# Optimization experiments

Measured on AMD Instinct MI355X. Metric: run time of the kernel, lower is better.

The kernel has to match this reference:

```python
import jax, jax.numpy as jnp
import numpy as np
import math

# ---- static configuration (mirrors Renderer defaults) ----
S = 129                                 # density cube side
L = math.ceil(S * math.sqrt(3))         # padded/rotation cube side = 224
C_ABS = 0.2                             # absorption coefficient c
LIGHTS = [
    {'dir': (2, 1, 1),    'rgb': (1.0, 69.0 / 255.0, 25.0 / 255.0)},
    {'dir': (-1, 0.5, 0), 'rgb': (227.0 / 255.0, 1.0, 66.0 / 255.0)},
]


def yp_from_light(l):
    ld = np.asarray(l, dtype=np.float64)
    ld = ld / np.sqrt(np.sum(ld ** 2))
    y = -math.asin(ld[0])
    if ld[2] < 0:
        y = -math.pi - y
    y = y * 180.0 / math.pi
    p = math.asin(ld[1]) * 180.0 / math.pi
    return y, p


def rot_matrix(yaw_deg, pitch_deg, order):
    # yaw about the y (height) axis, pitch about the x axis, roll = 0
    y = math.radians(yaw_deg)
    p = math.radians(pitch_deg)
    Ry = np.array([[math.cos(y), 0.0, math.sin(y)],
                   [0.0, 1.0, 0.0],
                   [-math.sin(y), 0.0, math.cos(y)]], dtype=np.float32)
    Rp = np.array([[1.0, 0.0, 0.0],
                   [0.0, math.cos(p), -math.sin(p)],
                   [0.0, math.sin(p), math.cos(p)]], dtype=np.float32)
    return Ry @ Rp if order == 'ypr' else Rp @ Ry

# base normalized sampling grid (align_corners=True convention), (x,y,z) order
_lin = np.linspace(-1.0, 1.0, L, dtype=np.float32)
_zz, _yy, _xx = np.meshgrid(_lin, _lin, _lin, indexing='ij')
BASE_XYZ = np.stack([_xx, _yy, _zz], axis=-1)   # [L,L,L,3]


def rotate_volume(vol, R):
    """Trilinear resampling of vol [B,C,D,H,W] under rotation R (zero padding)."""
    B, Ch, D, H, W = vol.shape
    src = jnp.einsum('dhwc,kc->dhwk', jnp.asarray(BASE_XYZ), jnp.asarray(R))
    xs = (src[..., 0] + 1.0) * 0.5 * (W - 1)
    ys = (src[..., 1] + 1.0) * 0.5 * (H - 1)
    zs = (src[..., 2] + 1.0) * 0.5 * (D - 1)
    x0 = jnp.floor(xs).astype(jnp.int32)
    y0 = jnp.floor(ys).astype(jnp.int32)
    z0 = jnp.floor(zs).astype(jnp.int32)
    wx = (xs - x0).astype(vol.dtype)
    wy = (ys - y0).astype(vol.dtype)
    wz = (zs - z0).astype(vol.dtype)
    flat = vol.reshape(B, Ch, D * H * W)

    def gather(zi, yi, xi):
        inb = ((zi >= 0) & (zi < D) & (yi >= 0) & (yi < H) & (xi >= 0) & (xi < W)).astype(vol.dtype)
        idx = ((jnp.clip(zi, 0, D - 1) * H + jnp.clip(yi, 0, H - 1)) * W
               + jnp.clip(xi, 0, W - 1)).reshape(-1)
        return jnp.take(flat, idx, axis=2).reshape(B, Ch, D, H, W) * inb

    out = (gather(z0,     y0,     x0)     * ((1 - wz) * (1 - wy) * (1 - wx))
         + gather(z0,     y0,     x0 + 1) * ((1 - wz) * (1 - wy) * wx)
         + gather(z0,     y0 + 1, x0)     * ((1 - wz) * wy * (1 - wx))
         + gather(z0,     y0 + 1, x0 + 1) * ((1 - wz) * wy * wx)
         + gather(z0 + 1, y0,     x0)     * (wz * (1 - wy) * (1 - wx))
         + gather(z0 + 1, y0,     x0 + 1) * (wz * (1 - wy) * wx)
         + gather(z0 + 1, y0 + 1, x0)     * (wz * wy * (1 - wx))
         + gather(z0 + 1, y0 + 1, x0 + 1) * (wz * wy * wx))
    return out


def _revcumsum(a):
    # torch.flip(cumsum(flip(a,[2]),2),[2]) : reverse cumulative sum along depth
    return jnp.flip(jnp.cumsum(jnp.flip(a, 2), axis=2), 2)


def setup_inputs() -> dict:
    key = jax.random.key(0)
    d = jax.random.uniform(key, (1, 1, S, S, S), dtype=jnp.float32)
    return {'d': d}


def reference(d):
    bs, _, Sd, _, _ = d.shape
    i = L // 2 - Sd // 2
    j = i + Sd
    light_array = jnp.zeros((bs, 3, Sd, Sd, Sd), dtype=d.dtype)
    for l in LIGHTS:
        y, p = yp_from_light(l['dir'])
        up = jnp.zeros((bs, 1, L, L, L), dtype=d.dtype).at[:, :, i:j, i:j, i:j].set(d)
        up = rotate_volume(up, rot_matrix(y, p, 'ypr'))
        up = jnp.exp(-C_ABS * _revcumsum(up))           # transmittance toward light
        up = rotate_volume(up, rot_matrix(-y, -p, 'rpy'))
        color = jnp.asarray(l['rgb'], dtype=d.dtype).reshape(1, 3, 1, 1, 1)
        light_array = light_array + up[:, :, i:j, i:j, i:j] * color
    t = jnp.exp(-C_ABS * _revcumsum(d))                  # view-ray transmittance
    out = C_ABS * jnp.sum(d * light_array * t, axis=2)   # background = 0
    return jnp.clip(out, 0.0, 1.0)
```

## Files before the change

kernel.cpp:

```cpp
#include <hip/hip_runtime.h>
#include <hip/hip_fp16.h>
#include <math.h>

#ifndef M_PI
#define M_PI 3.14159265358979323846
#endif

#define SS   129
#define LL   224
#define LL2  (LL*LL)
#define LL3  (LL*LL*LL)
#define SS2  (SS*SS)
#define SS3  (SS*SS*SS)
#define CABS 0.2f
#define PAD  48

#define BLO 45.5f
#define BHI 178.5f

#define NT1  28
#define NTZ16 14
#define ROTG  (2 * NTZ16 * 784)
#define ROTCH 392
#define NT3  17
#define NBZ16 9
#define BACKG (2 * NBZ16 * 289)
#define BACKCH 17
#define BACKG_P 5304
#define NTZ  28

#define NSEG 16
#define SEGZ 9
#define DSEGT (NSEG * SS2)
#define EXB1 ((DSEGT + 511) / 512)
#define EXB2 4
#define ROTG_E (ROTG + EXB1 + EXB2)
#define PREB1 ((DSEGT + 255) / 256)
#define SUFG (392 + PREB1)
#define TEXPB (2 * NTZ * LL2 / 2 / 256)

#define RBX 21
#define RBY 16
#define RBZ 18
#define RBN (RBX*RBY*RBZ)
#define RSXZ (RBX*RBZ)

#define BBX 21
#define BBY 16
#define BBZ 19
#define BBN (BBX*BBY*BBZ)
#define BSXZ (BBX*BBZ)

struct Mat3 { float m[9]; };
struct F3   { float x, y, z; };

__device__ __forceinline__ F3 tile_center(const Mat3& M, int ox, int oy, int oz) {
    float cbx = fmaf((float)ox + 3.5f, 2.0f / 223.0f, -1.0f);
    float cby = fmaf((float)oy + 3.5f, 2.0f / 223.0f, -1.0f);
    float cbz = fmaf((float)oz + 3.5f, 2.0f / 223.0f, -1.0f);
    F3 qc;
    qc.x = fmaf(fmaf(M.m[0], cbx, fmaf(M.m[1], cby, M.m[2] * cbz)), 111.5f, 111.5f);
    qc.y = fmaf(fmaf(M.m[3], cbx, fmaf(M.m[4], cby, M.m[5] * cbz)), 111.5f, 111.5f);
    qc.z = fmaf(fmaf(M.m[6], cbx, fmaf(M.m[7], cby, M.m[8] * cbz)), 111.5f, 111.5f);
    return qc;
}

__device__ __forceinline__ F3 tile_center16(const Mat3& M, int ox, int oy, int oz) {
    float cbx = fmaf((float)ox + 3.5f, 2.0f / 223.0f, -1.0f);
    float cby = fmaf((float)oy + 3.5f, 2.0f / 223.0f, -1.0f);
    float cbz = fmaf((float)oz + 7.5f, 2.0f / 223.0f, -1.0f);
    F3 qc;
    qc.x = fmaf(fmaf(M.m[0], cbx, fmaf(M.m[1], cby, M.m[2] * cbz)), 111.5f, 111.5f);
    qc.y = fmaf(fmaf(M.m[3], cbx, fmaf(M.m[4], cby, M.m[5] * cbz)), 111.5f, 111.5f);
    qc.z = fmaf(fmaf(M.m[6], cbx, fmaf(M.m[7], cby, M.m[8] * cbz)), 111.5f, 111.5f);
    return qc;
}

__device__ __forceinline__ bool tile_accept(F3 qc, F3 H) {
    return !(qc.x + H.x < BLO || qc.x - H.x > BHI ||
             qc.y + H.y < BLO || qc.y - H.y > BHI ||
             qc.z + H.z < BLO || qc.z - H.z > BHI);
}

__device__ __forceinline__ void qmap(const Mat3& M, int x, int y, int z,
                                     float& qx, float& qy, float& qz) {
    float bx = fmaf((float)x, 2.0f / 223.0f, -1.0f);
    float by = fmaf((float)y, 2.0f / 223.0f, -1.0f);
    float bz = fmaf((float)z, 2.0f / 223.0f, -1.0f);
    qx = fmaf(fmaf(M.m[0], bx, fmaf(M.m[1], by, M.m[2] * bz)), 111.5f, 111.5f);
    qy = fmaf(fmaf(M.m[3], bx, fmaf(M.m[4], by, M.m[5] * bz)), 111.5f, 111.5f);
    qz = fmaf(fmaf(M.m[6], bx, fmaf(M.m[7], by, M.m[8] * bz)), 111.5f, 111.5f);
}

__device__ __forceinline__ float fetch_d(const float* __restrict__ d, int z, int y, int x) {
    unsigned zz = (unsigned)(z - PAD), yy = (unsigned)(y - PAD), xx = (unsigned)(x - PAD);
    return (zz < (unsigned)SS && yy < (unsigned)SS && xx < (unsigned)SS)
        ? d[((int)zz * SS + (int)yy) * SS + (int)xx] : 0.0f;
}

__device__ __forceinline__ float fetch_T(const float* __restrict__ T, int z, int y, int x) {
    unsigned zz = (unsigned)z, yy = (unsigned)y, xx = (unsigned)x;
    return (zz < (unsigned)LL && yy < (unsigned)LL && xx < (unsigned)LL)
        ? T[((int)zz * LL + (int)yy) * LL + (int)xx] : 0.0f;
}

__device__ __forceinline__ float tri_T(const float* __restrict__ T, float qz, float qy, float qx) {
    int x0 = (int)floorf(qx), y0 = (int)floorf(qy), z0 = (int)floorf(qz);
    float wx = qx - (float)x0, wy = qy - (float)y0, wz = qz - (float)z0;
    float c000 = fetch_T(T, z0, y0, x0),     c001 = fetch_T(T, z0, y0, x0 + 1);
    float c010 = fetch_T(T, z0, y0 + 1, x0), c011 = fetch_T(T, z0, y0 + 1, x0 + 1);
    float c100 = fetch_T(T, z0 + 1, y0, x0),     c101 = fetch_T(T, z0 + 1, y0, x0 + 1);
    float c110 = fetch_T(T, z0 + 1, y0 + 1, x0), c111 = fetch_T(T, z0 + 1, y0 + 1, x0 + 1);
    float a00 = c000 + wx * (c001 - c000), a01 = c010 + wx * (c011 - c010);
    float a10 = c100 + wx * (c101 - c100), a11 = c110 + wx * (c111 - c110);
    float b0 = a00 + wy * (a01 - a00), b1 = a10 + wy * (a11 - a10);
    return b0 + wz * (b1 - b0);
}

__device__ __forceinline__ float tri_d_g(const float* __restrict__ d, float qz, float qy, float qx) {
    int x0 = (int)floorf(qx), y0 = (int)floorf(qy), z0 = (int)floorf(qz);
    float wx = qx - (float)x0, wy = qy - (float)y0, wz = qz - (float)z0;
    float c000 = fetch_d(d, z0, y0, x0),     c001 = fetch_d(d, z0, y0, x0 + 1);
    float c010 = fetch_d(d, z0, y0 + 1, x0), c011 = fetch_d(d, z0, y0 + 1, x0 + 1);
    float c100 = fetch_d(d, z0 + 1, y0, x0),     c101 = fetch_d(d, z0 + 1, y0, x0 + 1);
    float c110 = fetch_d(d, z0 + 1, y0 + 1, x0), c111 = fetch_d(d, z0 + 1, y0 + 1, x0 + 1);
    float a00 = c000 + wx * (c001 - c000), a01 = c010 + wx * (c011 - c010);
    float a10 = c100 + wx * (c101 - c100), a11 = c110 + wx * (c111 - c110);
    float b0 = a00 + wy * (a01 - a00), b1 = a10 + wy * (a11 - a10);
    return b0 + wz * (b1 - b0);
}

__device__ __forceinline__ float tri_rot(const float* __restrict__ S,
                                         float qx, float qy, float qz,
                                         int lox, int loy, int loz) {
    int x0 = (int)floorf(qx), y0 = (int)floorf(qy), z0 = (int)floorf(qz);
    float wx = qx - (float)x0, wy = qy - (float)y0, wz = qz - (float)z0;
    int i = (y0 - loy) * 378 + (z0 - loz) * 21 + (x0 - lox);
    float c000 = S[i],        c001 = S[i + 1];
    float cz0  = S[i + 21],   cz1  = S[i + 22];
    float cy0  = S[i + 378],  cy1  = S[i + 379];
    float cw0  = S[i + 399],  cw1  = S[i + 400];
    float a00 = c000 + wx * (c001 - c000);
    float a01 = cy0  + wx * (cy1  - cy0);
    float a10 = cz0  + wx * (cz1  - cz0);
    float a11 = cw0  + wx * (cw1  - cw0);
    float b0  = a00 + wy * (a01 - a00);
    float b1  = a10 + wy * (a11 - a10);
    return b0 + wz * (b1 - b0);
}

__device__ __forceinline__ float tri_back(const float* __restrict__ S,
                                          float qx, float qy, float qz,
                                          int lox, int loy, int loz) {
    int x0 = (int)floorf(qx), y0 = (int)floorf(qy), z0 = (int)floorf(qz);
    float wx = qx - (float)x0, wy = qy - (float)y0, wz = qz - (float)z0;
    int i = (y0 - loy) * 399 + (z0 - loz) * 21 + (x0 - lox);
    float c000 = S[i],        c001 = S[i + 1];
    float cz0  = S[i + 21],   cz1  = S[i + 22];
    float cy0  = S[i + 399],  cy1  = S[i + 400];
    float cw0  = S[i + 420],  cw1  = S[i + 421];
    float a00 = c000 + wx * (c001 - c000);
    float a01 = cy0  + wx * (cy1  - cy0);
    float a10 = cz0  + wx * (cz1  - cz0);
    float a11 = cw0  + wx * (cw1  - cw0);
    float b0  = a00 + wy * (a01 - a00);
    float b1  = a10 + wy * (a11 - a10);
    return b0 + wz * (b1 - b0);
}

__global__ __launch_bounds__(512) void k_rot(const float* __restrict__ d,
        __half* __restrict__ T0, __half* __restrict__ T1,
        float* __restrict__ S0, float* __restrict__ S1,
        float* __restrict__ Dseg, float* __restrict__ A,
        unsigned short* __restrict__ Run,
        Mat3 M0, Mat3 M1, F3 H0, F3 H1, F3 G0, F3 G1) {
    int n = blockIdx.x;
    int tid = threadIdx.x;
    if (n >= ROTG) {
        int e = n - ROTG;
        if (e < EXB1) {
            int t = e * 512 + tid;
            if (t < 2 * SS2) A[t] = 0.0f;
            if (t >= DSEGT) return;
            int seg = t / SS2, col = t - seg * SS2;
            int zs = seg * SEGZ, ze = min(SS, zs + SEGZ);
            float run = 0.0f;
            for (int z = zs; z < ze; ++z) run += d[z * SS2 + col];
            Dseg[t] = run;
        } else {
            int id = (e - EXB1) * 512 + tid;
            if (id >= 2 * 784) return;
            int l = id / 784, r = id - l * 784;
            int ty = r / 28, tx = r - ty * 28;
            const Mat3 M = l ? M1 : M0;
            const F3  G  = l ? G1 : G0;
            int t0 = -1, t1 = -1;
            for (int tz = 0; tz < NT1; ++tz) {
                F3 qc = tile_center(M, tx * 8, ty * 8, tz * 8);
                if (tile_accept(qc, G)) { if (t0 < 0) t0 = tz; t1 = tz; }
            }
            Run[id] = (t0 < 0) ? 0xFFFFu : (unsigned short)(t0 | (t1 << 8));
        }
        return;
    }

    int x8 = n & 7, i8 = n >> 3;
    int c = i8 / ROTCH, off = i8 - c * ROTCH;
    int b = (c * 8 + x8) * ROTCH + off;

    int light = b / (NTZ16 * 784);
    int r = b - light * (NTZ16 * 784);
    int tz16 = r / 784;
    int r2 = r - tz16 * 784;
    int tty = r2 / 28, ttx = r2 - tty * 28;

    const Mat3 M = light ? M1 : M0;
    const F3  H  = light ? H1 : H0;
    __half* __restrict__ T   = light ? T1 : T0;
    float* __restrict__ Ssum = light ? S1 : S0;

    int ox = ttx * 8, oy = tty * 8, oz = tz16 * 16;
    F3 qc = tile_center16(M, ox, oy, oz);
    if (!tile_accept(qc, H)) return;

    int lox = (int)floorf(qc.x - H.x);
    int loy = (int)floorf(qc.y - H.y);
    int loz = (int)floorf(qc.z - H.z);

    __shared__ float S[RBN];
    __shared__ float Sc[1024];

    if (tid < RSXZ) {
        int ix = tid % RBX, iz = tid / RBX;
        bool interior = (lox >= PAD) & (lox <= PAD + SS - RBX) &
                        (loy >= PAD) & (loy <= PAD + SS - RBY) &
                        (loz >= PAD) & (loz <= PAD + SS - RBZ);
        if (interior) {
            const float* g = d + ((size_t)(loz + iz - PAD) * SS + (loy - PAD)) * SS
                               + (lox + ix - PAD);
            #pragma unroll
            for (int j = 0; j < RBY; ++j)
                S[tid + j * RSXZ] = g[j * SS];
        } else {
            #pragma unroll
            for (int j = 0; j < RBY; ++j)
                S[tid + j * RSXZ] = fetch_d(d, loz + iz, loy + j, lox + ix);
        }
    }
    __syncthreads();

    int lx = tid & 7, ly = (tid >> 3) & 7, lz = tid >> 6;
    int col = tid & 63;
    float fx = (float)lx - 3.5f, fy = (float)ly - 3.5f, fz = (float)lz - 7.5f;
    float qx = qc.x + fmaf(M.m[0], fx, fmaf(M.m[1], fy, M.m[2] * fz));
    float qy = qc.y + fmaf(M.m[3], fx, fmaf(M.m[4], fy, M.m[5] * fz));
    float qz = qc.z + fmaf(M.m[6], fx, fmaf(M.m[7], fy, M.m[8] * fz));
    float v0 = tri_rot(S, qx, qy, qz, lox, loy, loz);
    float qx2 = qx + 8.0f * M.m[2];
    float qy2 = qy + 8.0f * M.m[5];
    float qz2 = qz + 8.0f * M.m[8];
    float v1 = tri_rot(S, qx2, qy2, qz2, lox, loy, loz);

    Sc[lz * 64 + col] = v0;
    Sc[(lz + 8) * 64 + col] = v1;
    __syncthreads();
    if (tid < 128) {
        int zz = tid >> 3, ly2 = tid & 7;
        const float4* Sc4 = (const float4*)Sc;
        float4 f0 = Sc4[zz * 16 + ly2 * 2];
        float4 f1 = Sc4[zz * 16 + ly2 * 2 + 1];
        union { __half2 h[4]; float4 v; } u;
        u.h[0] = __floats2half2_rn(f0.x, f0.y);
        u.h[1] = __floats2half2_rn(f0.z, f0.w);
        u.h[2] = __floats2half2_rn(f1.x, f1.y);
        u.h[3] = __floats2half2_rn(f1.z, f1.w);
        *(float4*)&T[(size_t)(oz + zz) * LL2 + (oy + ly2) * LL + ox] = u.v;
    } else if (tid < 256) {
        int t2 = tid - 128;
        int cc = t2 & 63, h = t2 >> 6;
        float s = 0.0f;
        #pragma unroll
        for (int k = 0; k < 8; ++k) s += Sc[(h * 8 + k) * 64 + cc];
        int so = (oy + (cc >> 3)) * LL + (ox + (cc & 7));
        Ssum[(2 * tz16 + h) * LL2 + so] = s;
    }
}

__global__ __launch_bounds__(256) void k_sufw(float* __restrict__ S0,
        float* __restrict__ S1, const unsigned short* __restrict__ Run,
        const float* __restrict__ d, const float* __restrict__ Dseg,
        __half* __restrict__ W) {
    int b = blockIdx.x;
    if (b < 392) {
        int l = b / 196;
        int col = (b - l * 196) * 256 + threadIdx.x;
        float* __restrict__ Ssum = l ? S1 : S0;
        int x = col % LL, y = col / LL;
        unsigned short r = Run[l * 784 + (y >> 3) * 28 + (x >> 3)];
        if (r == 0xFFFFu) return;
        int t0 = r & 0xFF, t1 = r >> 8;
        float vbuf[NTZ];
        #pragma unroll
        for (int t = 0; t < NTZ; ++t)
            vbuf[t] = (t >= t0 && t <= t1) ? Ssum[t * LL2 + col] : 0.0f;
        float run = 0.0f;
        #pragma unroll
        for (int t = NTZ - 1; t >= 0; --t) {
            if (t >= t0 && t <= t1) Ssum[t * LL2 + col] = run;
            run += vbuf[t];
        }
    } else {
        int t = (b - 392) * 256 + threadIdx.x;
        if (t >= DSEGT) return;
        int seg = t / SS2, col = t - seg * SS2;
        int zs = seg * SEGZ, ze = min(SS, zs + SEGZ);
        float run = 0.0f;
        for (int s2 = seg + 1; s2 < NSEG; ++s2) run += Dseg[s2 * SS2 + col];
        for (int z = ze - 1; z >= zs; --z) {
            float dv = d[z * SS2 + col];
            run += dv;
            W[z * SS2 + col] = __float2half(dv * __expf(-CABS * run));
        }
    }
}

__global__ __launch_bounds__(256) void k_texp(__half* __restrict__ T0,
        __half* __restrict__ T1, const float* __restrict__ S0,
        const float* __restrict__ S1, const unsigned short* __restrict__ Run) {
    int id = blockIdx.x * 256 + threadIdx.x;
    int light = id / (NTZ * LL2 / 2);
    int r = id - light * (NTZ * LL2 / 2);
    int t = r / (LL2 / 2), cp = r - t * (LL2 / 2);
    int col = cp * 2;
    int y = col / LL, x = col - y * LL;
    const unsigned short* Rl = Run + light * 784 + (y >> 3) * 28;
    unsigned short rtA = Rl[x >> 3];
    unsigned short rtB = Rl[(x + 1) >> 3];
    bool aA = (rtA != 0xFFFFu) && t >= (rtA & 0xFF) && t <= (rtA >> 8);
    bool aB = (rtB != 0xFFFFu) && t >= (rtB & 0xFF) && t <= (rtB >> 8);
    if (!aA && !aB) return;
    const float* __restrict__ Ssum = light ? S1 : S0;
    __half* __restrict__ T = light ? T1 : T0;
    float offA = aA ? Ssum[t * LL2 + col]     : 0.0f;
    float offB = aB ? Ssum[t * LL2 + col + 1] : 0.0f;
    __half2* Tp = (__half2*)(T + (size_t)(8 * t) * LL2 + col);
    float2 v[8];
    #pragma unroll
    for (int k = 0; k < 8; ++k) v[k] = __half22float2(Tp[k * (LL2 / 2)]);
    float sA = 0.0f, sB = 0.0f;
    #pragma unroll
    for (int k = 7; k >= 0; --k) { sA += v[k].x; sB += v[k].y; v[k].x = sA; v[k].y = sB; }
    #pragma unroll
    for (int k = 0; k < 8; ++k) {
        float eA = aA ? __expf(-CABS * (v[k].x + offA)) : v[k].x;
        float eB = aB ? __expf(-CABS * (v[k].y + offB)) : v[k].y;
        Tp[k * (LL2 / 2)] = __floats2half2_rn(eA, eB);
    }
}

template<bool BINT>
__global__ __launch_bounds__(512) void k_back(const __half* __restrict__ T0,
        const __half* __restrict__ T1, const __half* __restrict__ W,
        float* __restrict__ A0, float* __restrict__ A1,
        Mat3 M0, Mat3 M1, F3 H0, F3 H1) {
    int n = blockIdx.x;
    int x8 = n & 7, i8 = n >> 3;
    int c = i8 / BACKCH, off = i8 - c * BACKCH;
    int lb = (c * 8 + x8) * BACKCH + off;
    if (lb >= BACKG) return;

    int light = lb / (NBZ16 * 289); lb -= light * (NBZ16 * 289);
    int tz16 = lb / 289;
    int r2 = lb - tz16 * 289;
    int tty = r2 / 17, ttx = r2 - tty * 17;

    const Mat3 M = light ? M1 : M0;
    const F3  H  = light ? H1 : H0;
    const __half* __restrict__ T = light ? T1 : T0;
    float* __restrict__ A = light ? A1 : A0;

    int ox = ttx * 8, oy = tty * 8, oz = tz16 * 16;
    F3 qc = tile_center16(M, ox + PAD, oy + PAD, oz + PAD);
    int lox = (int)floorf(qc.x - H.x);
    int loy = (int)floorf(qc.y - H.y);
    int loz = (int)floorf(qc.z - H.z);

    __shared__ float S[BBN];
    __shared__ float Sc[512];
    int tid = threadIdx.x;

    if (tid < BSXZ) {
        int ix = tid % BBX, iz = tid / BBX;
        if (BINT) {
            const __half* tb = T + ((size_t)(loz + iz) * LL + loy) * LL + (lox + ix);
            #pragma unroll
            for (int j = 0; j < BBY; ++j)
                S[tid + j * BSXZ] = __half2float(tb[j * LL]);
        } else {
            #pragma unroll
            for (int j = 0; j < BBY; ++j) {
                int gz = loz + iz, gy = loy + j, gx = lox + ix;
                bool inb = ((unsigned)gz < (unsigned)LL) & ((unsigned)gy < (unsigned)LL)
                         & ((unsigned)gx < (unsigned)LL);
                S[tid + j * BSXZ] = inb
                    ? __half2float(T[((size_t)gz * LL + gy) * LL + gx]) : 0.0f;
            }
        }
    }
    __syncthreads();

    int lx = tid & 7, ly = (tid >> 3) & 7, lz = tid >> 6;
    int col = tid & 63;
    int x = ox + lx, y = oy + ly;
    float v0 = 0.0f, v1 = 0.0f;
    if (x < SS && y < SS) {
        float fx = (float)lx - 3.5f, fy = (float)ly - 3.5f, fz = (float)lz - 7.5f;
        float qx = qc.x + fmaf(M.m[0], fx, fmaf(M.m[1], fy, M.m[2] * fz));
        float qy = qc.y + fmaf(M.m[3], fx, fmaf(M.m[4], fy, M.m[5] * fz));
        float qz = qc.z + fmaf(M.m[6], fx, fmaf(M.m[7], fy, M.m[8] * fz));
        int z0 = oz + lz, z1 = oz + 8 + lz;
        if (z0 < SS)
            v0 = tri_back(S, qx, qy, qz, lox, loy, loz)
               * __half2float(W[(z0 * SS + y) * SS + x]);
        if (z1 < SS) {
            float qx2 = qx + 8.0f * M.m[2];
            float qy2 = qy + 8.0f * M.m[5];
            float qz2 = qz + 8.0f * M.m[8];
            v1 = tri_back(S, qx2, qy2, qz2, lox, loy, loz)
               * __half2float(W[(z1 * SS + y) * SS + x]);
        }
    }
    Sc[lz * 64 + col] = v0 + v1;
    __syncthreads();
    if (tid < 64) {
        float s = 0.0f;
        #pragma unroll
        for (int k = 0; k < 8; ++k) s += Sc[k * 64 + tid];
        int xx = ox + (tid & 7), yy = oy + (tid >> 3);
        if (xx < SS && yy < SS) atomicAdd(&A[yy * SS + xx], s);
    }
}

__global__ __launch_bounds__(256) void k_combine(const float* __restrict__ A0,
        const float* __restrict__ A1, float* __restrict__ out, F3 c0, F3 c1) {
    int i = blockIdx.x * 256 + threadIdx.x;
    if (i >= 3 * SS2) return;
    int ch = i / SS2, col = i - ch * SS2;
    float r0 = (ch == 0) ? c0.x : ((ch == 1) ? c0.y : c0.z);
    float r1 = (ch == 0) ? c1.x : ((ch == 1) ? c1.y : c1.z);
    float o = CABS * (A0[col] * r0 + A1[col] * r1);
    out[i] = fminf(fmaxf(o, 0.0f), 1.0f);
}

__global__ __launch_bounds__(256) void k_rot_full(const float* __restrict__ d,
                                                  float* __restrict__ T, Mat3 R) {
    int i = blockIdx.x * 256 + threadIdx.x;
    if (i >= LL3) return;
    int x = i % LL; int r = i / LL; int y = r % LL; int z = r / LL;
    float qx, qy, qz; qmap(R, x, y, z, qx, qy, qz);
    T[i] = tri_d_g(d, qz, qy, qx);
}

__global__ __launch_bounds__(256) void k_scan_full(float* __restrict__ T) {
    int col = blockIdx.x * 256 + threadIdx.x;
    if (col >= LL2) return;
    float run = 0.0f;
    for (int z = LL - 1; z >= 0; --z) {
        int idx = z * LL2 + col;
        run += T[idx];
        T[idx] = __expf(-CABS * run);
    }
}

__global__ __launch_bounds__(64) void k_fused_back(const float* __restrict__ T,
        const float* __restrict__ d, float* __restrict__ LA, Mat3 RT,
        float cr, float cg, float cb, int first) {
    int col = blockIdx.x * 64 + threadIdx.x;
    if (col >= SS2) return;
    int y = col / SS, x = col % SS;
    float run = 0.0f, acc = 0.0f;
    for (int z = SS - 1; z >= 0; --z) {
        float qx, qy, qz; qmap(RT, x + PAD, y + PAD, z + PAD, qx, qy, qz);
        float u = tri_T(T, qz, qy, qx);
        float dv = d[z * SS2 + col];
        run += dv;
        acc = fmaf(dv * __expf(-CABS * run), u, acc);
    }
    if (first) {
        LA[0 * SS2 + col] = acc * cr;
        LA[1 * SS2 + col] = acc * cg;
        LA[2 * SS2 + col] = acc * cb;
    } else {
        LA[0 * SS2 + col] += acc * cr;
        LA[1 * SS2 + col] += acc * cg;
        LA[2 * SS2 + col] += acc * cb;
    }
}

__global__ __launch_bounds__(256) void k_clip(const float* __restrict__ LA,
                                              float* __restrict__ out) {
    int i = blockIdx.x * 256 + threadIdx.x;
    if (i < 3 * SS2) out[i] = fminf(fmaxf(CABS * LA[i], 0.0f), 1.0f);
}

static void light_mats(const double ld_in[3], Mat3& R, Mat3& RT) {
    double n = sqrt(ld_in[0]*ld_in[0] + ld_in[1]*ld_in[1] + ld_in[2]*ld_in[2]);
    double l0 = ld_in[0]/n, l1 = ld_in[1]/n, l2 = ld_in[2]/n;
    double yv = -asin(l0);
    if (l2 < 0) yv = -M_PI - yv;
    double yd = yv * 180.0 / M_PI, pd = asin(l1) * 180.0 / M_PI;
    double yr = yd * M_PI / 180.0, pr = pd * M_PI / 180.0;
    float cy = (float)cos(yr), sy = (float)sin(yr), cp = (float)cos(pr), sp = (float)sin(pr);
    float m[9] = { cy,  sy*sp,  sy*cp,
                   0.f, cp,    -sp,
                  -sy,  cy*sp,  cy*cp };
    for (int i = 0; i < 9; ++i) R.m[i] = m[i];
    RT.m[0] = m[0]; RT.m[1] = m[3]; RT.m[2] = m[6];
    RT.m[3] = m[1]; RT.m[4] = m[4]; RT.m[5] = m[7];
    RT.m[6] = m[2]; RT.m[7] = m[5]; RT.m[8] = m[8];
}

static F3 half_span8(const Mat3& M) {
    F3 h;
    h.x = 3.5f * (fabsf(M.m[0]) + fabsf(M.m[1]) + fabsf(M.m[2])) + 0.05f;
    h.y = 3.5f * (fabsf(M.m[3]) + fabsf(M.m[4]) + fabsf(M.m[5])) + 0.05f;
    h.z = 3.5f * (fabsf(M.m[6]) + fabsf(M.m[7]) + fabsf(M.m[8])) + 0.05f;
    return h;
}

static F3 half_span16(const Mat3& M) {
    F3 h;
    h.x = 3.5f * (fabsf(M.m[0]) + fabsf(M.m[1])) + 7.5f * fabsf(M.m[2]) + 0.1f;
    h.y = 3.5f * (fabsf(M.m[3]) + fabsf(M.m[4])) + 7.5f * fabsf(M.m[5]) + 0.1f;
    h.z = 3.5f * (fabsf(M.m[6]) + fabsf(M.m[7])) + 7.5f * fabsf(M.m[8]) + 0.1f;
    return h;
}

static void h_qc16(const Mat3& M, double ox, double oy, double oz, double q[3]) {
    double cb[3] = { (ox + 3.5) * 2.0 / 223.0 - 1.0,
                     (oy + 3.5) * 2.0 / 223.0 - 1.0,
                     (oz + 7.5) * 2.0 / 223.0 - 1.0 };
    for (int k = 0; k < 3; ++k)
        q[k] = ((double)M.m[3*k] * cb[0] + (double)M.m[3*k+1] * cb[1]
              + (double)M.m[3*k+2] * cb[2]) * 111.5 + 111.5;
}

extern "C" void kernel_launch(void* const* d_in, const int* in_sizes, int n_in,
                              void* d_out, int out_size, void* d_ws, size_t ws_size,
                              hipStream_t stream) {
    const float* d = (const float*)d_in[0];
    float* out = (float*)d_out;

    const double dirs[2][3] = { {2.0, 1.0, 1.0}, {-1.0, 0.5, 0.0} };
    F3 c0 = { 1.0f, 69.0f / 255.0f, 25.0f / 255.0f };
    F3 c1 = { 227.0f / 255.0f, 1.0f, 66.0f / 255.0f };
    Mat3 R[2], RT[2];
    light_mats(dirs[0], R[0], RT[0]);
    light_mats(dirs[1], R[1], RT[1]);
    F3 H8[2]  = { half_span8(R[0]),  half_span8(R[1])  };
    F3 H16[2] = { half_span16(R[0]), half_span16(R[1]) };
    F3 HB[2]  = { half_span16(RT[0]), half_span16(RT[1]) };

    bool bint = true;
    for (int l = 0; l < 2 && bint; ++l) {
        double H[3] = { HB[l].x, HB[l].y, HB[l].z };
        int dim[3] = { BBX, BBY, BBZ };
        for (int tz = 0; tz < NBZ16 && bint; ++tz)
            for (int ty = 0; ty < NT3 && bint; ++ty)
                for (int tx = 0; tx < NT3; ++tx) {
                    double q[3]; h_qc16(RT[l], tx * 8 + PAD, ty * 8 + PAD, tz * 16 + PAD, q);
                    for (int k = 0; k < 3; ++k) {
                        int lo = (int)floor(q[k] - H[k]);
                        if (lo < 1 || lo + dim[k] > LL - 1) { bint = false; break; }
                    }
                    if (!bint) break;
                }
    }

    const size_t f32n = (size_t)(2 * NTZ * LL2 + NSEG * SS2 + 2 * SS2);
    const size_t need_A = f32n * 4 + (size_t)(SS3 + 2 * LL3) * 2 + 2 * 784 * 2;
    const size_t need_C = (size_t)(LL3 + 3 * SS2) * 4;

    if (ws_size >= need_A) {
        float* S0   = (float*)d_ws;
        float* S1   = S0 + NTZ * LL2;
        float* Dseg = S1 + NTZ * LL2;
        float* A0   = Dseg + NSEG * SS2;
        float* A1   = A0 + SS2;
        __half* W   = (__half*)(A1 + SS2);
        __half* T0  = W + SS3;
        __half* T1  = T0 + LL3;
        unsigned short* Run = (unsigned short*)(T1 + LL3);

        k_rot  <<<ROTG_E, 512, 0, stream>>>(d, T0, T1, S0, S1, Dseg, A0, Run,
                                            R[0], R[1], H16[0], H16[1], H8[0], H8[1]);
        k_sufw <<<SUFG, 256, 0, stream>>>(S0, S1, Run, d, Dseg, W);
        k_texp <<<TEXPB, 256, 0, stream>>>(T0, T1, S0, S1, Run);
        if (bint)
            k_back<true><<<BACKG_P, 512, 0, stream>>>(T0, T1, W, A0, A1,
                                                      RT[0], RT[1], HB[0], HB[1]);
        else
            k_back<false><<<BACKG_P, 512, 0, stream>>>(T0, T1, W, A0, A1,
                                                       RT[0], RT[1], HB[0], HB[1]);
        k_combine<<<(3 * SS2 + 255) / 256, 256, 0, stream>>>(A0, A1, out, c0, c1);
    } else if (ws_size >= need_C) {
        float* T  = (float*)d_ws;
        float* LA = T + LL3;
        for (int l = 0; l < 2; ++l) {
            k_rot_full <<<(LL3 + 255) / 256, 256, 0, stream>>>(d, T, R[l]);
            k_scan_full<<<(LL2 + 255) / 256, 256, 0, stream>>>(T);
            k_fused_back<<<(SS2 + 63) / 64, 64, 0, stream>>>(T, d, LA, RT[l],
                l ? c1.x : c0.x, l ? c1.y : c0.y, l ? c1.z : c0.z, l == 0);
        }
        k_clip<<<(3 * SS2 + 255) / 256, 256, 0, stream>>>(LA, out);
    }
}
```

Baseline: 166.0 us.

## Fuse pipeline into one cooperative persistent kernel with grid syncs

Replaces the five separate launches (rotate, suffix sums, texp, back-projection, combine) with a single cooperative kernel that uses grid-wide syncs between stages and persistent blocks looping over work. It aims to remove per-launch overhead and inter-kernel gaps. The trade-off is that occupancy is capped by cooperative residency, the block-to-tile mapping loses the earlier swizzled ordering, and the shared-memory footprint becomes the max across stages. The sufw scan loop is also simplified to iterate only the active tile range.

```diff
diff --git a/kernel.cpp b/kernel.cpp
--- a/kernel.cpp
+++ b/kernel.cpp
@@ -1,6 +1,9 @@
 #include <hip/hip_runtime.h>
 #include <hip/hip_fp16.h>
+#include <hip/hip_cooperative_groups.h>
 #include <math.h>
+
+namespace cg = cooperative_groups;
 
 #ifndef M_PI
 #define M_PI 3.14159265358979323846
@@ -166,6 +169,275 @@
     float b0  = a00 + wy * (a01 - a00);
     float b1  = a10 + wy * (a11 - a10);
     return b0 + wz * (b1 - b0);
+}
+
+__global__ __launch_bounds__(512) void k_all(const float* __restrict__ d,
+        __half* __restrict__ T0, __half* __restrict__ T1,
+        float* __restrict__ S0, float* __restrict__ S1,
+        float* __restrict__ Dseg, float* __restrict__ A0, float* __restrict__ A1,
+        __half* __restrict__ W, unsigned short* __restrict__ Run,
+        float* __restrict__ out,
+        Mat3 M0, Mat3 M1, Mat3 P0, Mat3 P1,
+        F3 H0, F3 H1, F3 G0, F3 G1, F3 B0, F3 B1,
+        F3 c0, F3 c1, int bint) {
+    cg::grid_group gg = cg::this_grid();
+    const int tid  = threadIdx.x;
+    const int nb   = gridDim.x;
+    const int gtid = blockIdx.x * 512 + tid;
+    const int gth  = nb * 512;
+
+    __shared__ float S[BBN];
+    __shared__ float Sc[1024];
+
+    for (int t = gtid; t < 2 * SS2; t += gth) A0[t] = 0.0f;
+    for (int t = gtid; t < DSEGT; t += gth) {
+        int seg = t / SS2, col = t - seg * SS2;
+        int zs = seg * SEGZ, ze = min(SS, zs + SEGZ);
+        float run = 0.0f;
+        for (int z = zs; z < ze; ++z) run += d[z * SS2 + col];
+        Dseg[t] = run;
+    }
+    for (int id = gtid; id < 2 * 784; id += gth) {
+        int l = id / 784, r = id - l * 784;
+        int ty = r / 28, tx = r - ty * 28;
+        const Mat3 M = l ? M1 : M0;
+        const F3  G  = l ? G1 : G0;
+        int t0 = -1, t1 = -1;
+        for (int tz = 0; tz < NT1; ++tz) {
+            F3 qc = tile_center(M, tx * 8, ty * 8, tz * 8);
+            if (tile_accept(qc, G)) { if (t0 < 0) t0 = tz; t1 = tz; }
+        }
+        Run[id] = (t0 < 0) ? 0xFFFFu : (unsigned short)(t0 | (t1 << 8));
+    }
+
+    {
+        int bch = (ROTG + nb - 1) / nb;
+        int base = blockIdx.x * bch;
+        for (int k = 0; k < bch; ++k) {
+            int b = base + k;
+            if (b >= ROTG) break;
+            int light = b / (NTZ16 * 784);
+            int r = b - light * (NTZ16 * 784);
+            int tz16 = r / 784;
+            int r2 = r - tz16 * 784;
+            int tty = r2 / 28, ttx = r2 - tty * 28;
+
+            const Mat3 M = light ? M1 : M0;
+            const F3  H  = light ? H1 : H0;
+            __half* __restrict__ T   = light ? T1 : T0;
+            float* __restrict__ Ssum = light ? S1 : S0;
+
+            int ox = ttx * 8, oy = tty * 8, oz = tz16 * 16;
+            F3 qc = tile_center16(M, ox, oy, oz);
+            if (!tile_accept(qc, H)) continue;
+
+            int lox = (int)floorf(qc.x - H.x);
+            int loy = (int)floorf(qc.y - H.y);
+            int loz = (int)floorf(qc.z - H.z);
+
+            if (tid < RSXZ) {
+                int ix = tid % RBX, iz = tid / RBX;
+                bool interior = (lox >= PAD) & (lox <= PAD + SS - RBX) &
+                                (loy >= PAD) & (loy <= PAD + SS - RBY) &
+                                (loz >= PAD) & (loz <= PAD + SS - RBZ);
+                if (interior) {
+                    const float* g = d + ((size_t)(loz + iz - PAD) * SS + (loy - PAD)) * SS
+                                       + (lox + ix - PAD);
+                    #pragma unroll
+                    for (int j = 0; j < RBY; ++j)
+                        S[tid + j * RSXZ] = g[j * SS];
+                } else {
+                    #pragma unroll
+                    for (int j = 0; j < RBY; ++j)
+                        S[tid + j * RSXZ] = fetch_d(d, loz + iz, loy + j, lox + ix);
+                }
+            }
+            __syncthreads();
+
+            int lx = tid & 7, ly = (tid >> 3) & 7, lz = tid >> 6;
+            int col = tid & 63;
+            float fx = (float)lx - 3.5f, fy = (float)ly - 3.5f, fz = (float)lz - 7.5f;
+            float qx = qc.x + fmaf(M.m[0], fx, fmaf(M.m[1], fy, M.m[2] * fz));
+            float qy = qc.y + fmaf(M.m[3], fx, fmaf(M.m[4], fy, M.m[5] * fz));
+            float qz = qc.z + fmaf(M.m[6], fx, fmaf(M.m[7], fy, M.m[8] * fz));
+            float v0 = tri_rot(S, qx, qy, qz, lox, loy, loz);
+            float qx2 = qx + 8.0f * M.m[2];
+            float qy2 = qy + 8.0f * M.m[5];
+            float qz2 = qz + 8.0f * M.m[8];
+            float v1 = tri_rot(S, qx2, qy2, qz2, lox, loy, loz);
+
+            Sc[lz * 64 + col] = v0;
+            Sc[(lz + 8) * 64 + col] = v1;
+            __syncthreads();
+            if (tid < 128) {
+                int zz = tid >> 3, ly2 = tid & 7;
+                const float4* Sc4 = (const float4*)Sc;
+                float4 f0 = Sc4[zz * 16 + ly2 * 2];
+                float4 f1 = Sc4[zz * 16 + ly2 * 2 + 1];
+                union { __half2 h[4]; float4 v; } u;
+                u.h[0] = __floats2half2_rn(f0.x, f0.y);
+                u.h[1] = __floats2half2_rn(f0.z, f0.w);
+                u.h[2] = __floats2half2_rn(f1.x, f1.y);
+                u.h[3] = __floats2half2_rn(f1.z, f1.w);
+                *(float4*)&T[(size_t)(oz + zz) * LL2 + (oy + ly2) * LL + ox] = u.v;
+            } else if (tid < 256) {
+                int t2 = tid - 128;
+                int cc = t2 & 63, h = t2 >> 6;
+                float s = 0.0f;
+                #pragma unroll
+                for (int kk = 0; kk < 8; ++kk) s += Sc[(h * 8 + kk) * 64 + cc];
+                int so = (oy + (cc >> 3)) * LL + (ox + (cc & 7));
+                Ssum[(2 * tz16 + h) * LL2 + so] = s;
+            }
+            __syncthreads();
+        }
+    }
+    gg.sync();
+
+    for (int i = gtid; i < 2 * LL2; i += gth) {
+        int l = i / LL2, col = i - l * LL2;
+        float* __restrict__ Ssum = l ? S1 : S0;
+        int x = col % LL, y = col / LL;
+        unsigned short r = Run[l * 784 + (y >> 3) * 28 + (x >> 3)];
+        if (r == 0xFFFFu) continue;
+        int t0 = r & 0xFF, t1 = r >> 8;
+        float run = 0.0f;
+        for (int t = t1; t >= t0; --t) {
+            float v = Ssum[t * LL2 + col];
+            Ssum[t * LL2 + col] = run;
+            run += v;
+        }
+    }
+    for (int t = gtid; t < DSEGT; t += gth) {
+        int seg = t / SS2, col = t - seg * SS2;
+        int zs = seg * SEGZ, ze = min(SS, zs + SEGZ);
+        float run = 0.0f;
+        for (int s2 = seg + 1; s2 < NSEG; ++s2) run += Dseg[s2 * SS2 + col];
+        for (int z = ze - 1; z >= zs; --z) {
+            float dv = d[z * SS2 + col];
+            run += dv;
+            W[z * SS2 + col] = __float2half(dv * __expf(-CABS * run));
+        }
+    }
+    gg.sync();
+
+    for (int id = gtid; id < NTZ * LL2; id += gth) {
+        int light = id / (NTZ * LL2 / 2);
+        int r = id - light * (NTZ * LL2 / 2);
+        int t = r / (LL2 / 2), cp = r - t * (LL2 / 2);
+        int col = cp * 2;
+        int y = col / LL, x = col - y * LL;
+        const unsigned short* Rl = Run + light * 784 + (y >> 3) * 28;
+        unsigned short rtA = Rl[x >> 3];
+        unsigned short rtB = Rl[(x + 1) >> 3];
+        bool aA = (rtA != 0xFFFFu) && t >= (rtA & 0xFF) && t <= (rtA >> 8);
+        bool aB = (rtB != 0xFFFFu) && t >= (rtB & 0xFF) && t <= (rtB >> 8);
+        if (!aA && !aB) continue;
+        const float* __restrict__ Ssum = light ? S1 : S0;
+        __half* __restrict__ T = light ? T1 : T0;
+        float offA = aA ? Ssum[t * LL2 + col]     : 0.0f;
+        float offB = aB ? Ssum[t * LL2 + col + 1] : 0.0f;
+        __half2* Tp = (__half2*)(T + (size_t)(8 * t) * LL2 + col);
+        float2 v[8];
+        #pragma unroll
+        for (int k = 0; k < 8; ++k) v[k] = __half22float2(Tp[k * (LL2 / 2)]);
+        float sA = 0.0f, sB = 0.0f;
+        #pragma unroll
+        for (int k = 7; k >= 0; --k) { sA += v[k].x; sB += v[k].y; v[k].x = sA; v[k].y = sB; }
+        #pragma unroll
+        for (int k = 0; k < 8; ++k) {
+            float eA = aA ? __expf(-CABS * (v[k].x + offA)) : v[k].x;
+            float eB = aB ? __expf(-CABS * (v[k].y + offB)) : v[k].y;
+            Tp[k * (LL2 / 2)] = __floats2half2_rn(eA, eB);
+        }
+    }
+    gg.sync();
+
+    {
+        int ech = (BACKG + nb - 1) / nb;
+        int base = blockIdx.x * ech;
+        for (int k = 0; k < ech; ++k) {
+            int b = base + k;
+            if (b >= BACKG) break;
+            int light = b / (NBZ16 * 289);
+            int lb = b - light * (NBZ16 * 289);
+            int tz16 = lb / 289;
+            int r2 = lb - tz16 * 289;
+            int tty = r2 / 17, ttx = r2 - tty * 17;
+
+            const Mat3 M = light ? P1 : P0;
+            const F3  H  = light ? B1 : B0;
+            const __half* __restrict__ T = light ? T1 : T0;
+            float* __restrict__ A = light ? A1 : A0;
+
+            int ox = ttx * 8, oy = tty * 8, oz = tz16 * 16;
+            F3 qc = tile_center16(M, ox + PAD, oy + PAD, oz + PAD);
+            int lox = (int)floorf(qc.x - H.x);
+            int loy = (int)floorf(qc.y - H.y);
+            int loz = (int)floorf(qc.z - H.z);
+
+            if (tid < BSXZ) {
+                int ix = tid % BBX, iz = tid / BBX;
+                if (bint) {
+                    const __half* tb = T + ((size_t)(loz + iz) * LL + loy) * LL + (lox + ix);
+                    #pragma unroll
+                    for (int j = 0; j < BBY; ++j)
+                        S[tid + j * BSXZ] = __half2float(tb[j * LL]);
+                } else {
+                    #pragma unroll
+                    for (int j = 0; j < BBY; ++j) {
+                        int gz = loz + iz, gy = loy + j, gx = lox + ix;
+                        bool inb = ((unsigned)gz < (unsigned)LL) & ((unsigned)gy < (unsigned)LL)
+                                 & ((unsigned)gx < (unsigned)LL);
+                        S[tid + j * BSXZ] = inb
+                            ? __half2float(T[((size_t)gz * LL + gy) * LL + gx]) : 0.0f;
+                    }
+                }
+            }
+            __syncthreads();
+
+            int lx = tid & 7, ly = (tid >> 3) & 7, lz = tid >> 6;
+            int col = tid & 63;
+            int x = ox + lx, y = oy + ly;
+            float v0 = 0.0f, v1 = 0.0f;
+            if (x < SS && y < SS) {
+                float fx = (float)lx - 3.5f, fy = (float)ly - 3.5f, fz = (float)lz - 7.5f;
+                float qx = qc.x + fmaf(M.m[0], fx, fmaf(M.m[1], fy, M.m[2] * fz));
+                float qy = qc.y + fmaf(M.m[3], fx, fmaf(M.m[4], fy, M.m[5] * fz));
+                float qz = qc.z + fmaf(M.m[6], fx, fmaf(M.m[7], fy, M.m[8] * fz));
+                int z0 = oz + lz, z1 = oz + 8 + lz;
+                if (z0 < SS)
+                    v0 = tri_back(S, qx, qy, qz, lox, loy, loz)
+                       * __half2float(W[(z0 * SS + y) * SS + x]);
+                if (z1 < SS) {
+                    float qx2 = qx + 8.0f * M.m[2];
+                    float qy2 = qy + 8.0f * M.m[5];
+                    float qz2 = qz + 8.0f * M.m[8];
+                    v1 = tri_back(S, qx2, qy2, qz2, lox, loy, loz)
+                       * __half2float(W[(z1 * SS + y) * SS + x]);
+                }
+            }
+            Sc[lz * 64 + col] = v0 + v1;
+            __syncthreads();
+            if (tid < 64) {
+                float s = 0.0f;
+                #pragma unroll
+                for (int kk = 0; kk < 8; ++kk) s += Sc[kk * 64 + tid];
+                int xx = ox + (tid & 7), yy = oy + (tid >> 3);
+                if (xx < SS && yy < SS) atomicAdd(&A[yy * SS + xx], s);
+            }
+            __syncthreads();
+        }
+    }
+    gg.sync();
+
+    for (int i = gtid; i < 3 * SS2; i += gth) {
+        int ch = i / SS2, col = i - ch * SS2;
+        float r0 = (ch == 0) ? c0.x : ((ch == 1) ? c0.y : c0.z);
+        float r1 = (ch == 0) ? c1.x : ((ch == 1) ? c1.y : c1.z);
+        float o = CABS * (A0[col] * r0 + A1[col] * r1);
+        out[i] = fminf(fmaxf(o, 0.0f), 1.0f);
+    }
 }
 
 __global__ __launch_bounds__(512) void k_rot(const float* __restrict__ d,
@@ -203,33 +475,26 @@
         }
         return;
     }
-
     int x8 = n & 7, i8 = n >> 3;
     int c = i8 / ROTCH, off = i8 - c * ROTCH;
     int b = (c * 8 + x8) * ROTCH + off;
-
     int light = b / (NTZ16 * 784);
     int r = b - light * (NTZ16 * 784);
     int tz16 = r / 784;
     int r2 = r - tz16 * 784;
     int tty = r2 / 28, ttx = r2 - tty * 28;
-
     const Mat3 M = light ? M1 : M0;
     const F3  H  = light ? H1 : H0;
     __half* __restrict__ T   = light ? T1 : T0;
     float* __restrict__ Ssum = light ? S1 : S0;
-
     int ox = ttx * 8, oy = tty * 8, oz = tz16 * 16;
     F3 qc = tile_center16(M, ox, oy, oz);
     if (!tile_accept(qc, H)) return;
-
     int lox = (int)floorf(qc.x - H.x);
     int loy = (int)floorf(qc.y - H.y);
     int loz = (int)floorf(qc.z - H.z);
-
     __shared__ float S[RBN];
     __shared__ float Sc[1024];
-
     if (tid < RSXZ) {
         int ix = tid % RBX, iz = tid / RBX;
         bool interior = (lox >= PAD) & (lox <= PAD + SS - RBX) &
@@ -248,7 +513,6 @@
         }
     }
     __syncthreads();
-
     int lx = tid & 7, ly = (tid >> 3) & 7, lz = tid >> 6;
     int col = tid & 63;
     float fx = (float)lx - 3.5f, fy = (float)ly - 3.5f, fz = (float)lz - 7.5f;
@@ -260,7 +524,6 @@
     float qy2 = qy + 8.0f * M.m[5];
     float qz2 = qz + 8.0f * M.m[8];
     float v1 = tri_rot(S, qx2, qy2, qz2, lox, loy, loz);
-
     Sc[lz * 64 + col] = v0;
     Sc[(lz + 8) * 64 + col] = v1;
     __syncthreads();
@@ -299,15 +562,11 @@
         unsigned short r = Run[l * 784 + (y >> 3) * 28 + (x >> 3)];
         if (r == 0xFFFFu) return;
         int t0 = r & 0xFF, t1 = r >> 8;
-        float vbuf[NTZ];
-        #pragma unroll
-        for (int t = 0; t < NTZ; ++t)
-            vbuf[t] = (t >= t0 && t <= t1) ? Ssum[t * LL2 + col] : 0.0f;
         float run = 0.0f;
-        #pragma unroll
-        for (int t = NTZ - 1; t >= 0; --t) {
-            if (t >= t0 && t <= t1) Ssum[t * LL2 + col] = run;
-            run += vbuf[t];
+        for (int t = t1; t >= t0; --t) {
+            float v = Ssum[t * LL2 + col];
+            Ssum[t * LL2 + col] = run;
+            run += v;
         }
     } else {
         int t = (b - 392) * 256 + threadIdx.x;
@@ -368,27 +627,22 @@
     int c = i8 / BACKCH, off = i8 - c * BACKCH;
     int lb = (c * 8 + x8) * BACKCH + off;
     if (lb >= BACKG) return;
-
     int light = lb / (NBZ16 * 289); lb -= light * (NBZ16 * 289);
     int tz16 = lb / 289;
     int r2 = lb - tz16 * 289;
     int tty = r2 / 17, ttx = r2 - tty * 17;
-
     const Mat3 M = light ? M1 : M0;
     const F3  H  = light ? H1 : H0;
     const __half* __restrict__ T = light ? T1 : T0;
     float* __restrict__ A = light ? A1 : A0;
-
     int ox = ttx * 8, oy = tty * 8, oz = tz16 * 16;
     F3 qc = tile_center16(M, ox + PAD, oy + PAD, oz + PAD);
     int lox = (int)floorf(qc.x - H.x);
     int loy = (int)floorf(qc.y - H.y);
     int loz = (int)floorf(qc.z - H.z);
-
     __shared__ float S[BBN];
     __shared__ float Sc[512];
     int tid = threadIdx.x;
-
     if (tid < BSXZ) {
         int ix = tid % BBX, iz = tid / BBX;
         if (BINT) {
@@ -408,7 +662,6 @@
         }
     }
     __syncthreads();
-
     int lx = tid & 7, ly = (tid >> 3) & 7, lz = tid >> 6;
     int col = tid & 63;
     int x = ox + lx, y = oy + ly;
@@ -474,7 +727,7 @@
 
 __global__ __launch_bounds__(64) void k_fused_back(const float* __restrict__ T,
         const float* __restrict__ d, float* __restrict__ LA, Mat3 RT,
-        float cr, float cg, float cb, int first) {
+        float cr, float cg2, float cb, int first) {
     int col = blockIdx.x * 64 + threadIdx.x;
     if (col >= SS2) return;
     int y = col / SS, x = col % SS;
@@ -488,11 +741,11 @@
     }
     if (first) {
         LA[0 * SS2 + col] = acc * cr;
-        LA[1 * SS2 + col] = acc * cg;
+        LA[1 * SS2 + col] = acc * cg2;
         LA[2 * SS2 + col] = acc * cb;
     } else {
         LA[0 * SS2 + col] += acc * cr;
-        LA[1 * SS2 + col] += acc * cg;
+        LA[1 * SS2 + col] += acc * cg2;
         LA[2 * SS2 + col] += acc * cb;
     }
 }
@@ -592,17 +845,49 @@
         __half* T1  = T0 + LL3;
         unsigned short* Run = (unsigned short*)(T1 + LL3);
 
-        k_rot  <<<ROTG_E, 512, 0, stream>>>(d, T0, T1, S0, S1, Dseg, A0, Run,
-                                            R[0], R[1], H16[0], H16[1], H8[0], H8[1]);
-        k_sufw <<<SUFG, 256, 0, stream>>>(S0, S1, Run, d, Dseg, W);
-        k_texp <<<TEXPB, 256, 0, stream>>>(T0, T1, S0, S1, Run);
-        if (bint)
-            k_back<true><<<BACKG_P, 512, 0, stream>>>(T0, T1, W, A0, A1,
-                                                      RT[0], RT[1], HB[0], HB[1]);
-        else
-            k_back<false><<<BACKG_P, 512, 0, stream>>>(T0, T1, W, A0, A1,
-                                                       RT[0], RT[1], HB[0], HB[1]);
-        k_combine<<<(3 * SS2 + 255) / 256, 256, 0, stream>>>(A0, A1, out, c0, c1);
+        static int coop = -1;
+        static int gridN = 0;
+        if (coop < 0) {
+            int dev = 0;
+            hipGetDevice(&dev);
+            int attr = 0;
+            hipDeviceGetAttribute(&attr, hipDeviceAttributeCooperativeLaunch, dev);
+            hipDeviceProp_t prop;
+            hipGetDeviceProperties(&prop, dev);
+            int nbk = 0;
+            hipOccupancyMaxActiveBlocksPerMultiprocessor(&nbk, k_all, 512, 0);
+            gridN = nbk * prop.multiProcessorCount;
+            coop = (attr && gridN > 0) ? 1 : 0;
+        }
+
+        bool done = false;
+        if (coop == 1) {
+            int bintI = bint ? 1 : 0;
+            void* args[] = { (void*)&d, (void*)&T0, (void*)&T1, (void*)&S0, (void*)&S1,
+                             (void*)&Dseg, (void*)&A0, (void*)&A1, (void*)&W, (void*)&Run,
+                             (void*)&out,
+                             (void*)&R[0], (void*)&R[1], (void*)&RT[0], (void*)&RT[1],
+                             (void*)&H16[0], (void*)&H16[1], (void*)&H8[0], (void*)&H8[1],
+                             (void*)&HB[0], (void*)&HB[1], (void*)&c0, (void*)&c1,
+                             (void*)&bintI };
+            hipError_t e = hipLaunchCooperativeKernel(k_all, dim3(gridN), dim3(512),
+                                                      args, 0, stream);
+            done = (e == hipSuccess);
+            if (!done) coop = 0;
+        }
+        if (!done) {
+            k_rot  <<<ROTG_E, 512, 0, stream>>>(d, T0, T1, S0, S1, Dseg, A0, Run,
+                                                R[0], R[1], H16[0], H16[1], H8[0], H8[1]);
+            k_sufw <<<SUFG, 256, 0, stream>>>(S0, S1, Run, d, Dseg, W);
+            k_texp <<<TEXPB, 256, 0, stream>>>(T0, T1, S0, S1, Run);
+            if (bint)
+                k_back<true><<<BACKG_P, 512, 0, stream>>>(T0, T1, W, A0, A1,
+                                                          RT[0], RT[1], HB[0], HB[1]);
+            else
+                k_back<false><<<BACKG_P, 512, 0, stream>>>(T0, T1, W, A0, A1,
+                                                           RT[0], RT[1], HB[0], HB[1]);
+            k_combine<<<(3 * SS2 + 255) / 256, 256, 0, stream>>>(A0, A1, out, c0, c1);
+        }
     } else if (ws_size >= need_C) {
         float* T  = (float*)d_ws;
         float* LA = T + LL3;
```

New measurement: 562.3 us. +238.7%, slower.

## Fuse depth scan and exp into a single per-column sequential pass

Applied to the files above, without the earlier changes.

Replaces the block-partial-sum approach (k_rot writing 8-slice partial sums, k_sufw suffix-scanning them, k_texp applying offsets and exp) with one kernel in which each thread walks its column pair from back to front, carrying a running sum and writing exp-transmittance directly. This removes the S0/S1 float buffers, their global traffic and one kernel launch. The extra rotation blocks are moved to the front of the grid, and the W buffer is padded to keep T0 aligned. The trade-off is less parallelism in the scan: only 2*LL2/2 threads each loop serially over up to 28 tiles, which may leave the GPU underoccupied and raise latency.

```diff
diff --git a/kernel.cpp b/kernel.cpp
--- a/kernel.cpp
+++ b/kernel.cpp
@@ -9,6 +9,7 @@
 #define SS   129
 #define LL   224
 #define LL2  (LL*LL)
+#define LLH  (LL2/2)
 #define LL3  (LL*LL*LL)
 #define SS2  (SS*SS)
 #define SS3  (SS*SS*SS)
@@ -34,10 +35,11 @@
 #define DSEGT (NSEG * SS2)
 #define EXB1 ((DSEGT + 511) / 512)
 #define EXB2 4
-#define ROTG_E (ROTG + EXB1 + EXB2)
+#define EXB  (EXB1 + EXB2)
+#define ROTG_E (ROTG + EXB)
+#define TXB  (2 * LLH / 256)
 #define PREB1 ((DSEGT + 255) / 256)
-#define SUFG (392 + PREB1)
-#define TEXPB (2 * NTZ * LL2 / 2 / 256)
+#define MIDG (TXB + PREB1)
 
 #define RBX 21
 #define RBY 16
@@ -170,16 +172,14 @@
 
 __global__ __launch_bounds__(512) void k_rot(const float* __restrict__ d,
         __half* __restrict__ T0, __half* __restrict__ T1,
-        float* __restrict__ S0, float* __restrict__ S1,
         float* __restrict__ Dseg, float* __restrict__ A,
         unsigned short* __restrict__ Run,
         Mat3 M0, Mat3 M1, F3 H0, F3 H1, F3 G0, F3 G1) {
     int n = blockIdx.x;
     int tid = threadIdx.x;
-    if (n >= ROTG) {
-        int e = n - ROTG;
-        if (e < EXB1) {
-            int t = e * 512 + tid;
+    if (n < EXB) {
+        if (n < EXB1) {
+            int t = n * 512 + tid;
             if (t < 2 * SS2) A[t] = 0.0f;
             if (t >= DSEGT) return;
             int seg = t / SS2, col = t - seg * SS2;
@@ -188,7 +188,7 @@
             for (int z = zs; z < ze; ++z) run += d[z * SS2 + col];
             Dseg[t] = run;
         } else {
-            int id = (e - EXB1) * 512 + tid;
+            int id = (n - EXB1) * 512 + tid;
             if (id >= 2 * 784) return;
             int l = id / 784, r = id - l * 784;
             int ty = r / 28, tx = r - ty * 28;
@@ -204,7 +204,8 @@
         return;
     }
 
-    int x8 = n & 7, i8 = n >> 3;
+    int nn = n - EXB;
+    int x8 = nn & 7, i8 = nn >> 3;
     int c = i8 / ROTCH, off = i8 - c * ROTCH;
     int b = (c * 8 + x8) * ROTCH + off;
 
@@ -216,8 +217,7 @@
 
     const Mat3 M = light ? M1 : M0;
     const F3  H  = light ? H1 : H0;
-    __half* __restrict__ T   = light ? T1 : T0;
-    float* __restrict__ Ssum = light ? S1 : S0;
+    __half* __restrict__ T = light ? T1 : T0;
 
     int ox = ttx * 8, oy = tty * 8, oz = tz16 * 16;
     F3 qc = tile_center16(M, ox, oy, oz);
@@ -275,42 +275,44 @@
         u.h[2] = __floats2half2_rn(f1.x, f1.y);
         u.h[3] = __floats2half2_rn(f1.z, f1.w);
         *(float4*)&T[(size_t)(oz + zz) * LL2 + (oy + ly2) * LL + ox] = u.v;
-    } else if (tid < 256) {
-        int t2 = tid - 128;
-        int cc = t2 & 63, h = t2 >> 6;
-        float s = 0.0f;
-        #pragma unroll
-        for (int k = 0; k < 8; ++k) s += Sc[(h * 8 + k) * 64 + cc];
-        int so = (oy + (cc >> 3)) * LL + (ox + (cc & 7));
-        Ssum[(2 * tz16 + h) * LL2 + so] = s;
-    }
-}
-
-__global__ __launch_bounds__(256) void k_sufw(float* __restrict__ S0,
-        float* __restrict__ S1, const unsigned short* __restrict__ Run,
+    }
+}
+
+__global__ __launch_bounds__(256) void k_mid(__half* __restrict__ T0,
+        __half* __restrict__ T1, const unsigned short* __restrict__ Run,
         const float* __restrict__ d, const float* __restrict__ Dseg,
         __half* __restrict__ W) {
     int b = blockIdx.x;
-    if (b < 392) {
-        int l = b / 196;
-        int col = (b - l * 196) * 256 + threadIdx.x;
-        float* __restrict__ Ssum = l ? S1 : S0;
-        int x = col % LL, y = col / LL;
-        unsigned short r = Run[l * 784 + (y >> 3) * 28 + (x >> 3)];
-        if (r == 0xFFFFu) return;
-        int t0 = r & 0xFF, t1 = r >> 8;
-        float vbuf[NTZ];
-        #pragma unroll
-        for (int t = 0; t < NTZ; ++t)
-            vbuf[t] = (t >= t0 && t <= t1) ? Ssum[t * LL2 + col] : 0.0f;
-        float run = 0.0f;
-        #pragma unroll
-        for (int t = NTZ - 1; t >= 0; --t) {
-            if (t >= t0 && t <= t1) Ssum[t * LL2 + col] = run;
-            run += vbuf[t];
+    if (b < TXB) {
+        int id = b * 256 + threadIdx.x;
+        int light = id / LLH;
+        int cp = id - light * LLH;
+        int col = cp * 2;
+        int y = col / LL, x = col - y * LL;
+        unsigned short rt = Run[light * 784 + (y >> 3) * 28 + (x >> 3)];
+        if (rt == 0xFFFFu) return;
+        int t0 = rt & 0xFF, t1 = rt >> 8;
+        __half2* __restrict__ Tp = (__half2*)(light ? T1 : T0) + cp;
+        float runA = 0.0f, runB = 0.0f;
+        for (int t = t1; t >= t0; --t) {
+            __half2* Tt = Tp + (size_t)(8 * t) * LLH;
+            float2 v[8];
+            #pragma unroll
+            for (int k = 0; k < 8; ++k) v[k] = __half22float2(Tt[k * LLH]);
+            float a = runA, bb = runB;
+            #pragma unroll
+            for (int k = 7; k >= 0; --k) {
+                a += v[k].x; bb += v[k].y;
+                v[k].x = a;  v[k].y = bb;
+            }
+            runA = a; runB = bb;
+            #pragma unroll
+            for (int k = 0; k < 8; ++k)
+                Tt[k * LLH] = __floats2half2_rn(__expf(-CABS * v[k].x),
+                                                __expf(-CABS * v[k].y));
         }
     } else {
-        int t = (b - 392) * 256 + threadIdx.x;
+        int t = (b - TXB) * 256 + threadIdx.x;
         if (t >= DSEGT) return;
         int seg = t / SS2, col = t - seg * SS2;
         int zs = seg * SEGZ, ze = min(SS, zs + SEGZ);
@@ -321,40 +323,6 @@
             run += dv;
             W[z * SS2 + col] = __float2half(dv * __expf(-CABS * run));
         }
-    }
-}
-
-__global__ __launch_bounds__(256) void k_texp(__half* __restrict__ T0,
-        __half* __restrict__ T1, const float* __restrict__ S0,
-        const float* __restrict__ S1, const unsigned short* __restrict__ Run) {
-    int id = blockIdx.x * 256 + threadIdx.x;
-    int light = id / (NTZ * LL2 / 2);
-    int r = id - light * (NTZ * LL2 / 2);
-    int t = r / (LL2 / 2), cp = r - t * (LL2 / 2);
-    int col = cp * 2;
-    int y = col / LL, x = col - y * LL;
-    const unsigned short* Rl = Run + light * 784 + (y >> 3) * 28;
-    unsigned short rtA = Rl[x >> 3];
-    unsigned short rtB = Rl[(x + 1) >> 3];
-    bool aA = (rtA != 0xFFFFu) && t >= (rtA & 0xFF) && t <= (rtA >> 8);
-    bool aB = (rtB != 0xFFFFu) && t >= (rtB & 0xFF) && t <= (rtB >> 8);
-    if (!aA && !aB) return;
-    const float* __restrict__ Ssum = light ? S1 : S0;
-    __half* __restrict__ T = light ? T1 : T0;
-    float offA = aA ? Ssum[t * LL2 + col]     : 0.0f;
-    float offB = aB ? Ssum[t * LL2 + col + 1] : 0.0f;
-    __half2* Tp = (__half2*)(T + (size_t)(8 * t) * LL2 + col);
-    float2 v[8];
-    #pragma unroll
-    for (int k = 0; k < 8; ++k) v[k] = __half22float2(Tp[k * (LL2 / 2)]);
-    float sA = 0.0f, sB = 0.0f;
-    #pragma unroll
-    for (int k = 7; k >= 0; --k) { sA += v[k].x; sB += v[k].y; v[k].x = sA; v[k].y = sB; }
-    #pragma unroll
-    for (int k = 0; k < 8; ++k) {
-        float eA = aA ? __expf(-CABS * (v[k].x + offA)) : v[k].x;
-        float eB = aB ? __expf(-CABS * (v[k].y + offB)) : v[k].y;
-        Tp[k * (LL2 / 2)] = __floats2half2_rn(eA, eB);
     }
 }
 
@@ -577,25 +545,23 @@
                 }
     }
 
-    const size_t f32n = (size_t)(2 * NTZ * LL2 + NSEG * SS2 + 2 * SS2);
-    const size_t need_A = f32n * 4 + (size_t)(SS3 + 2 * LL3) * 2 + 2 * 784 * 2;
+    const size_t f32n = (size_t)(NSEG * SS2 + 2 * SS2);
+    const size_t ss3p = ((size_t)SS3 + 7) & ~(size_t)7;
+    const size_t need_A = f32n * 4 + (ss3p + 2 * LL3) * 2 + 2 * 784 * 2;
     const size_t need_C = (size_t)(LL3 + 3 * SS2) * 4;
 
     if (ws_size >= need_A) {
-        float* S0   = (float*)d_ws;
-        float* S1   = S0 + NTZ * LL2;
-        float* Dseg = S1 + NTZ * LL2;
+        float* Dseg = (float*)d_ws;
         float* A0   = Dseg + NSEG * SS2;
         float* A1   = A0 + SS2;
         __half* W   = (__half*)(A1 + SS2);
-        __half* T0  = W + SS3;
+        __half* T0  = W + ss3p;
         __half* T1  = T0 + LL3;
         unsigned short* Run = (unsigned short*)(T1 + LL3);
 
-        k_rot  <<<ROTG_E, 512, 0, stream>>>(d, T0, T1, S0, S1, Dseg, A0, Run,
+        k_rot  <<<ROTG_E, 512, 0, stream>>>(d, T0, T1, Dseg, A0, Run,
                                             R[0], R[1], H16[0], H16[1], H8[0], H8[1]);
-        k_sufw <<<SUFG, 256, 0, stream>>>(S0, S1, Run, d, Dseg, W);
-        k_texp <<<TEXPB, 256, 0, stream>>>(T0, T1, S0, S1, Run);
+        k_mid  <<<MIDG, 256, 0, stream>>>(T0, T1, Run, d, Dseg, W);
         if (bint)
             k_back<true><<<BACKG_P, 512, 0, stream>>>(T0, T1, W, A0, A1,
                                                       RT[0], RT[1], HB[0], HB[1]);
```

Result: slower. 173.5 us (+4.5%).
